# Kernel tuning notes

Hardware: AMD Instinct MI355X
Metric: run time of the kernel (lower is better)

Reference implementation:

```python
import jax, jax.numpy as jnp
import numpy as np

N_NODES = 10000
N_EDGES = 160000
N_GRAPHS = 64
F = 80        # hidden dim
T = 5         # towers
F_OUT = 16    # per-tower post output (80/5)
N_LAYERS = 4
EPS = 1e-6
BN_EPS = 1e-5
STD_EPS = 1e-5


def setup_inputs() -> dict:
    key = jax.random.key(0)
    ks = jax.random.split(key, 12)
    x = jax.random.uniform(ks[0], (N_NODES, 2), dtype=jnp.float32)
    edge_index = jax.random.randint(ks[1], (2, N_EDGES), 0, N_NODES, dtype=jnp.int64)
    batch = jnp.sort(jax.random.randint(ks[2], (N_NODES,), 0, N_GRAPHS, dtype=jnp.int64))

    def w(k, shape, fan_in):
        return (jax.random.normal(k, shape, jnp.float32) / np.float32(np.sqrt(fan_in)))

    return {
        "x": x, "edge_index": edge_index, "batch": batch,
        "pre_lin_W": w(ks[3], (1, F), 1), "pre_lin_b": jnp.zeros((F,), jnp.float32),
        "pre_W": w(ks[4], (N_LAYERS, T, 2 * F, F), 2 * F), "pre_b": jnp.zeros((N_LAYERS, T, F), jnp.float32),
        "post_W": w(ks[5], (N_LAYERS, T, 13 * F, F_OUT), 13 * F), "post_b": jnp.zeros((N_LAYERS, T, F_OUT), jnp.float32),
        "lin_W": w(ks[6], (N_LAYERS, F, F), F), "lin_b": jnp.zeros((N_LAYERS, F), jnp.float32),
        "bn_gamma": jnp.ones((N_LAYERS, F), jnp.float32), "bn_beta": jnp.zeros((N_LAYERS, F), jnp.float32),
        "mlp_lin_W": w(ks[7], (40, 1), 40), "mlp_lin_b": jnp.zeros((1,), jnp.float32),
        "mlp1_W": w(ks[8], (40, 20), 40), "mlp1_b": jnp.zeros((20,), jnp.float32),
        "mlp2_W": w(ks[9], (20, 1), 20), "mlp2_b": jnp.zeros((1,), jnp.float32),
    }


def _pna_conv(h, src, dst, deg, avg_log_deg, preW, preb, postW, postb, linW, linb):
    # h: [N, F]; messages per tower: pre MLP over cat(x_i, x_j)  (divide_input=False)
    N = h.shape[0]
    hm = jnp.concatenate([h[dst], h[src]], axis=-1)            # [E, 2F]
    m = jnp.einsum('ef,tfo->eto', hm, preW) + preb             # [E, T, F]

    cnt = jnp.maximum(deg, 1.0)[:, None, None]                 # [N,1,1]
    has = (deg > 0)[:, None, None]
    s = jax.ops.segment_sum(m, dst, num_segments=N)
    mean = s / cnt
    mean_sq = jax.ops.segment_sum(m * m, dst, num_segments=N) / cnt
    mn = jax.ops.segment_min(m, dst, num_segments=N)
    mx = jax.ops.segment_max(m, dst, num_segments=N)
    mn = jnp.where(has, mn, 0.0)
    mx = jnp.where(has, mx, 0.0)
    std = jnp.sqrt(jax.nn.relu(mean_sq - mean * mean) + STD_EPS)
    agg = jnp.concatenate([mean, mn, mx, std], axis=-1)        # [N, T, 4F]

    logd = jnp.log(jnp.maximum(deg, 1.0) + 1.0)[:, None, None]
    amp = agg * (logd / avg_log_deg)
    att = agg * (avg_log_deg / logd)
    out = jnp.concatenate([agg, amp, att], axis=-1)            # [N, T, 12F]

    xt = jnp.broadcast_to(h[:, None, :], (N, T, F))
    out = jnp.concatenate([xt, out], axis=-1)                  # [N, T, 13F]
    out = jnp.einsum('ntf,tfo->nto', out, postW) + postb       # [N, T, F_OUT]
    out = out.reshape(N, T * F_OUT)                            # [N, 80]
    return out @ linW + linb


def _forward(x, edge_index, batch, pre_lin_W, pre_lin_b, pre_W, pre_b,
             post_W, post_b, lin_W, lin_b, bn_gamma, bn_beta,
             mlp_lin_W, mlp_lin_b, mlp1_W, mlp1_b, mlp2_W, mlp2_b):
    N = x.shape[0]
    src, dst = edge_index[0], edge_index[1]
    deg = jax.ops.segment_sum(jnp.ones_like(dst, jnp.float32), dst, num_segments=N)
    avg_log_deg = jnp.mean(jnp.log(deg + 1.0))                 # PNA avg log-degree from deg histogram

    operation = x[:, 0:1]
    assignment = x[:, 1:2]
    op = operation @ pre_lin_W + pre_lin_b                     # [N, 80]

    for l in range(N_LAYERS):
        y = _pna_conv(op, src, dst, deg, avg_log_deg,
                      pre_W[l], pre_b[l], post_W[l], post_b[l], lin_W[l], lin_b[l])
        mu = jnp.mean(y, axis=0)
        var = jnp.mean((y - mu) ** 2, axis=0)                  # biased, training-mode BN
        y = (y - mu) / jnp.sqrt(var + BN_EPS) * bn_gamma[l] + bn_beta[l]
        op = jax.nn.relu(y)

    front, behind = op[:, :40], op[:, 40:]
    xc = front * assignment + behind                           # [N, 40], non-negative

    # LastLayer: log-space scatter-add message passing
    log_score = jax.ops.segment_sum(jnp.log(xc[src] + EPS), dst, num_segments=N)
    xc = jnp.exp(log_score + jnp.log(xc + EPS))

    # global mean pool over graphs
    gcnt = jnp.maximum(jax.ops.segment_sum(jnp.ones_like(batch, jnp.float32), batch, num_segments=N_GRAPHS), 1.0)
    pooled = jax.ops.segment_sum(xc, batch, num_segments=N_GRAPHS) / gcnt[:, None]  # [B, 40]

    x_lin = pooled @ mlp_lin_W + mlp_lin_b
    x_cv = pooled @ mlp1_W + mlp1_b
    x_cv = 20.0 - jax.nn.relu(x_cv)
    x_cv = x_cv @ mlp2_W + mlp2_b
    return x_cv + x_lin                                        # [B, 1]


def reference(x, edge_index, batch, pre_lin_W, pre_lin_b, pre_W, pre_b,
              post_W, post_b, lin_W, lin_b, bn_gamma, bn_beta,
              mlp_lin_W, mlp_lin_b, mlp1_W, mlp1_b, mlp2_W, mlp2_b):
    return _forward(x, edge_index, batch, pre_lin_W, pre_lin_b, pre_W, pre_b,
                    post_W, post_b, lin_W, lin_b, bn_gamma, bn_beta,
                    mlp_lin_W, mlp_lin_b, mlp1_W, mlp1_b, mlp2_W, mlp2_b)
```

## Files before the change

### kernel.cpp

```cpp
#include <hip/hip_runtime.h>
#include <math.h>

#define NN 10000
#define NE 160000
#define NG 64
#define FEAT 80
#define NT 5
#define NL 4

__global__ void k_cnt2(const int* __restrict__ dst, const int* __restrict__ batch,
                       int* __restrict__ deg, int* __restrict__ gcnt) {
    int e = blockIdx.x * 256 + threadIdx.x;
    if (e < NE) atomicAdd(&deg[dst[e]], 1);
    if (e < NN) atomicAdd(&gcnt[batch[e]], 1);
}

__global__ void k_scan(const int* __restrict__ deg, int* __restrict__ offs) {
    __shared__ int sums[256];
    int tid = threadIdx.x;
    int start = tid * 40, stop = min(start + 40, NN);
    int s = 0;
    for (int i = start; i < stop; ++i) s += deg[i];
    sums[tid] = s;
    __syncthreads();
    for (int off = 1; off < 256; off <<= 1) {
        int v = (tid >= off) ? sums[tid - off] : 0;
        __syncthreads();
        sums[tid] += v;
        __syncthreads();
    }
    int base = (tid == 0) ? 0 : sums[tid - 1];
    for (int i = start; i < stop; ++i) { offs[i] = base; base += deg[i]; }
    if (tid == 255) offs[NN] = sums[255];
}

__global__ void k_ald(const int* __restrict__ deg, float* __restrict__ ald) {
    __shared__ float red[256];
    int i = blockIdx.x * 256 + threadIdx.x;
    red[threadIdx.x] = (i < NN) ? logf((float)deg[i] + 1.0f) : 0.0f;
    __syncthreads();
    for (int s = 128; s > 0; s >>= 1) {
        if (threadIdx.x < s) red[threadIdx.x] += red[threadIdx.x + s];
        __syncthreads();
    }
    if (threadIdx.x == 0) atomicAdd(ald, red[0]);
}

__global__ void k_fill(const int* __restrict__ src, const int* __restrict__ dst,
                       const int* __restrict__ offs, int* __restrict__ cursor,
                       int* __restrict__ csr) {
    int e = blockIdx.x * 256 + threadIdx.x;
    if (e < NE) {
        int d = dst[e];
        int p = atomicAdd(&cursor[d], 1);
        csr[offs[d] + p] = src[e];
    }
}

__global__ void k_op0(const float* __restrict__ x, const float* __restrict__ plW,
                      const float* __restrict__ plb, float* __restrict__ hT) {
    int i = blockIdx.x * 256 + threadIdx.x;
    if (i < FEAT * NN) {
        int f = i / NN, n = i - f * NN;
        hT[i] = x[2 * n] * plW[f] + plb[f];
    }
}

__global__ __launch_bounds__(256) void k_mm_ab(
        const float* __restrict__ hT_in, const float* __restrict__ preW_l,
        float* __restrict__ A, float* __restrict__ Bt,
        const float* __restrict__ yT, const float* __restrict__ bnst_p,
        const float* __restrict__ gamma_p, const float* __restrict__ beta_p,
        float* __restrict__ hT_out, int use_bn) {
    __shared__ float hs[16][80];
    int n0 = blockIdx.x * 16;
    int tid = threadIdx.x;
    for (int i = tid; i < 16 * 80; i += 256) {
        int nl = i & 15, f = i >> 4;
        float v;
        if (use_bn) {
            float y = yT[(size_t)f * NN + n0 + nl];
            float mu = bnst_p[f] * (1.f / NN);
            float msq = bnst_p[80 + f] * (1.f / NN);
            float var = fmaxf(msq - mu * mu, 0.f);
            v = (y - mu) * (1.f / sqrtf(var + 1e-5f)) * gamma_p[f] + beta_p[f];
            v = fmaxf(v, 0.f);
            hT_out[(size_t)f * NN + n0 + nl] = v;
        } else {
            v = hT_in[(size_t)f * NN + n0 + nl];
        }
        hs[nl][f] = v;
    }
    __syncthreads();
    float acc[4][16];
#pragma unroll
    for (int s = 0; s < 4; s++)
#pragma unroll
        for (int i = 0; i < 16; i++) acc[s][i] = 0.f;
    const float* wp[4];
#pragma unroll
    for (int s = 0; s < 4; s++) {
        int c = tid + s * 256;
        int cs = (c < 800) ? c : 0;
        int part = (cs >= 400) ? 1 : 0;
        int cc = cs - part * 400;
        int t = cc / 80, o = cc - t * 80;
        wp[s] = preW_l + (size_t)(t * 160 + part * 80) * 80 + o;
    }
    for (int fq = 0; fq < 80; fq += 4) {
        float w[4][4];
#pragma unroll
        for (int s = 0; s < 4; s++) {
            w[s][0] = wp[s][(fq + 0) * 80];
            w[s][1] = wp[s][(fq + 1) * 80];
            w[s][2] = wp[s][(fq + 2) * 80];
            w[s][3] = wp[s][(fq + 3) * 80];
        }
#pragma unroll
        for (int i = 0; i < 16; i++) {
            float4 hv = *(const float4*)&hs[i][fq];
#pragma unroll
            for (int s = 0; s < 4; s++) {
                acc[s][i] += hv.x * w[s][0] + hv.y * w[s][1] +
                             hv.z * w[s][2] + hv.w * w[s][3];
            }
        }
    }
#pragma unroll
    for (int s = 0; s < 4; s++) {
        int c = tid + s * 256;
        if (c < 800) {
            int part = (c >= 400) ? 1 : 0;
            int cc = c - part * 400;
            int t = cc / 80, o = cc - t * 80;
            if (part == 0) {
#pragma unroll
                for (int i = 0; i < 16; i++) A[(size_t)(n0 + i) * 400 + cc] = acc[s][i];
            } else {
#pragma unroll
                for (int i = 0; i < 16; i++)
                    Bt[((size_t)t * NN + n0 + i) * 80 + o] = acc[s][i];
            }
        }
    }
}

__global__ __launch_bounds__(256) void k_agg_t(
        const float* __restrict__ A, const float* __restrict__ Bt,
        const int* __restrict__ offs, const int* __restrict__ csr,
        const float* __restrict__ preb_l, float* __restrict__ aggT) {
    __shared__ float st[320 * 17];
    int tid = threadIdx.x;
    int id = blockIdx.y * 625 + blockIdx.x;
    int xcd = id & 7;
    int slot = id >> 3;
    int base = (xcd <= 5) ? xcd * 391 : 5 * 391 + (xcd - 5) * 390;
    int r = base + slot;
    int t = r / 625;
    int n0 = (r - t * 625) * 16;
    int ni = tid >> 4;
    int cl = tid & 15;
    int n = n0 + ni;
    int e0 = offs[n], e1 = offs[n + 1];
    const float* Bts = Bt + (size_t)t * NN * 80;
    float s[5], q[5], mn[5], mx[5];
#pragma unroll
    for (int k = 0; k < 5; k++) { s[k] = 0.f; q[k] = 0.f; mn[k] = 3.4e38f; mx[k] = -3.4e38f; }
    int e = e0;
    for (; e + 3 < e1; e += 4) {
        const float* br0 = Bts + (size_t)csr[e] * 80 + cl;
        const float* br1 = Bts + (size_t)csr[e + 1] * 80 + cl;
        const float* br2 = Bts + (size_t)csr[e + 2] * 80 + cl;
        const float* br3 = Bts + (size_t)csr[e + 3] * 80 + cl;
#pragma unroll
        for (int k = 0; k < 5; k++) {
            float b0 = br0[k * 16];
            float b1 = br1[k * 16];
            float b2 = br2[k * 16];
            float b3 = br3[k * 16];
            s[k] += (b0 + b1) + (b2 + b3);
            q[k] += (b0 * b0 + b1 * b1) + (b2 * b2 + b3 * b3);
            mn[k] = fminf(mn[k], fminf(fminf(b0, b1), fminf(b2, b3)));
            mx[k] = fmaxf(mx[k], fmaxf(fmaxf(b0, b1), fmaxf(b2, b3)));
        }
    }
    for (; e < e1; ++e) {
        const float* br = Bts + (size_t)csr[e] * 80 + cl;
#pragma unroll
        for (int k = 0; k < 5; k++) {
            float b = br[k * 16];
            s[k] += b; q[k] += b * b;
            mn[k] = fminf(mn[k], b); mx[k] = fmaxf(mx[k], b);
        }
    }
    int d = e1 - e0;
    float degf = (float)d;
    float cnt = fmaxf(degf, 1.f);
#pragma unroll
    for (int k = 0; k < 5; k++) {
        int c = cl + k * 16;
        float a = A[(size_t)n * 400 + t * 80 + c] + preb_l[t * 80 + c];
        float mean = (degf * a + s[k]) / cnt;
        float msq  = (degf * a * a + 2.f * a * s[k] + q[k]) / cnt;
        float sd = sqrtf(fmaxf(msq - mean * mean, 0.f) + 1e-5f);
        float mnr = (d > 0) ? a + mn[k] : 0.f;
        float mxr = (d > 0) ? a + mx[k] : 0.f;
        st[(0 * 80 + c) * 17 + ni] = mean;
        st[(1 * 80 + c) * 17 + ni] = mnr;
        st[(2 * 80 + c) * 17 + ni] = mxr;
        st[(3 * 80 + c) * 17 + ni] = sd;
    }
    __syncthreads();
    int jj = tid >> 4;
    int nl = tid & 15;
#pragma unroll
    for (int pass = 0; pass < 20; ++pass) {
        int j = pass * 16 + jj;
        aggT[((size_t)t * 320 + j) * NN + n0 + nl] = st[j * 17 + nl];
    }
}

__global__ __launch_bounds__(256) void k_post(
        const float* __restrict__ hT, const float* __restrict__ aggT,
        const float* __restrict__ postW_l, const float* __restrict__ postb_l,
        const int* __restrict__ offs, const float* __restrict__ ald_sum,
        float* __restrict__ y0T) {
    __shared__ float wj[40 * 48];
    __shared__ float wh[80 * 16];
    int tid = threadIdx.x;
    int t = blockIdx.y;
    int jq = blockIdx.z;
    int j0 = jq * 40;
    const float* W0 = postW_l + (size_t)t * 1040 * 16;
    const float* W1 = W0 + 80 * 16;
    const float* W2 = W0 + 400 * 16;
    const float* W3 = W0 + 720 * 16;
    for (int idx = tid; idx < 40 * 48; idx += 256) {
        int j = idx / 48;
        int rem = idx - j * 48;
        int p = rem >> 4, o = rem & 15;
        const float* Wp = (p == 0) ? W1 : (p == 1) ? W2 : W3;
        wj[idx] = Wp[(j0 + j) * 16 + o];
    }
    if (jq == 0) {
        for (int idx = tid; idx < 80 * 16; idx += 256)
            wh[idx] = W0[idx];
    }
    __syncthreads();
    int n = blockIdx.x * 256 + tid;
    bool alive = (n < NN);
    int nc = alive ? n : 0;
    float acc1[16], acc2[16], acc3[16];
#pragma unroll
    for (int i = 0; i < 16; i++) { acc1[i] = 0.f; acc2[i] = 0.f; acc3[i] = 0.f; }
    const float* ap = aggT + ((size_t)t * 320 + j0) * NN + nc;
#pragma unroll 8
    for (int j = 0; j < 40; ++j) {
        float a = ap[(size_t)j * NN];
        const float* w = wj + j * 48;
#pragma unroll
        for (int i = 0; i < 16; i++) {
            acc1[i] += a * w[i];
            acc2[i] += a * w[16 + i];
            acc3[i] += a * w[32 + i];
        }
    }
    if (jq == 0) {
#pragma unroll 4
        for (int f = 0; f < 80; ++f) {
            float hv = hT[(size_t)f * NN + nc];
            const float* w = wh + f * 16;
#pragma unroll
            for (int i = 0; i < 16; i++) acc1[i] += hv * w[i];
        }
    }
    if (alive) {
        float degf = (float)(offs[n + 1] - offs[n]);
        float ald = ald_sum[0] * (1.f / NN);
        float logd = logf(fmaxf(degf, 1.f) + 1.f);
        float c1 = logd / ald;
        float c2 = ald / logd;
#pragma unroll
        for (int i = 0; i < 16; i++) {
            float v = acc1[i] + c1 * acc2[i] + c2 * acc3[i];
            if (jq == 0) v += postb_l[t * 16 + i];
            unsafeAtomicAdd(&y0T[(size_t)(t * 16 + i) * NN + n], v);
        }
    }
}

__global__ __launch_bounds__(256) void k_lin(
        const float* __restrict__ y0T, const float* __restrict__ linW_l,
        const float* __restrict__ linb_l, float* __restrict__ yT) {
    __shared__ float ws[80 * 8];
    int tid = threadIdx.x;
    int f0 = blockIdx.y * 8;
    for (int idx = tid; idx < 80 * 8; idx += 256)
        ws[idx] = linW_l[(idx >> 3) * 80 + f0 + (idx & 7)];
    __syncthreads();
    int n = blockIdx.x * 256 + tid;
    bool alive = (n < NN);
    int nc = alive ? n : 0;
    float acc[8];
#pragma unroll
    for (int i = 0; i < 8; i++) acc[i] = 0.f;
#pragma unroll 8
    for (int k = 0; k < 80; ++k) {
        float v = y0T[(size_t)k * NN + nc];
        const float4 wa = *(const float4*)(ws + k * 8);
        const float4 wb = *(const float4*)(ws + k * 8 + 4);
        acc[0] += v * wa.x; acc[1] += v * wa.y; acc[2] += v * wa.z; acc[3] += v * wa.w;
        acc[4] += v * wb.x; acc[5] += v * wb.y; acc[6] += v * wb.z; acc[7] += v * wb.w;
    }
    if (alive) {
#pragma unroll
        for (int i = 0; i < 8; i++)
            yT[(size_t)(f0 + i) * NN + n] = acc[i] + linb_l[f0 + i];
    }
}

__global__ void k_bnstats(const float* __restrict__ yT, float* __restrict__ bnst) {
    __shared__ float r1[256], r2[256];
    int f = blockIdx.x;
    int seg = blockIdx.y;
    int tid = threadIdx.x;
    int i0 = seg * 1250, i1 = min(i0 + 1250, NN);
    float s = 0.f, q = 0.f;
    for (int i = i0 + tid; i < i1; i += 256) {
        float v = yT[(size_t)f * NN + i];
        s += v; q += v * v;
    }
    r1[tid] = s; r2[tid] = q;
    __syncthreads();
    for (int st = 128; st > 0; st >>= 1) {
        if (tid < st) { r1[tid] += r1[tid + st]; r2[tid] += r2[tid + st]; }
        __syncthreads();
    }
    if (tid == 0) {
        unsafeAtomicAdd(&bnst[f], r1[0]);
        unsafeAtomicAdd(&bnst[80 + f], r2[0]);
    }
}

__global__ void k_bnxc(const float* __restrict__ yT, const float* __restrict__ bnst,
                       const float* __restrict__ gamma_l, const float* __restrict__ beta_l,
                       const float* __restrict__ x, float* __restrict__ lxc) {
    int i = blockIdx.x * 256 + threadIdx.x;
    if (i >= 40 * NN) return;
    int f = i / NN, n = i - f * NN;
    int f2 = f + 40;
    float mu1 = bnst[f] * (1.f / NN);
    float ms1 = bnst[80 + f] * (1.f / NN);
    float v1 = (yT[(size_t)f * NN + n] - mu1) *
               (1.f / sqrtf(fmaxf(ms1 - mu1 * mu1, 0.f) + 1e-5f)) * gamma_l[f] + beta_l[f];
    v1 = fmaxf(v1, 0.f);
    float mu2 = bnst[f2] * (1.f / NN);
    float ms2 = bnst[80 + f2] * (1.f / NN);
    float v2 = (yT[(size_t)f2 * NN + n] - mu2) *
               (1.f / sqrtf(fmaxf(ms2 - mu2 * mu2, 0.f) + 1e-5f)) * gamma_l[f2] + beta_l[f2];
    v2 = fmaxf(v2, 0.f);
    lxc[(size_t)n * 40 + f] = logf(v1 * x[2 * n + 1] + v2 + 1e-6f);
}

__global__ void k_logagg(const float* __restrict__ lxc, const int* __restrict__ offs,
                         const int* __restrict__ csr, const int* __restrict__ batch,
                         float* __restrict__ pooled) {
    int n = blockIdx.x;
    int tid = threadIdx.x;
    if (tid >= 40) return;
    int e0 = offs[n], e1 = offs[n + 1];
    float s = 0.f;
    for (int k = e0; k < e1; ++k) s += lxc[(size_t)csr[k] * 40 + tid];
    float v = expf(s + lxc[(size_t)n * 40 + tid]);
    atomicAdd(&pooled[batch[n] * 40 + tid], v);
}

__global__ void k_final(const float* __restrict__ pooled, const int* __restrict__ gcnt,
                        const float* __restrict__ mlW, const float* __restrict__ mlb,
                        const float* __restrict__ m1W, const float* __restrict__ m1b,
                        const float* __restrict__ m2W, const float* __restrict__ m2b,
                        float* __restrict__ out) {
    int g = threadIdx.x;
    if (g >= NG) return;
    float inv = 1.f / fmaxf((float)gcnt[g], 1.f);
    float pl[40];
#pragma unroll
    for (int j = 0; j < 40; j++) pl[j] = pooled[g * 40 + j] * inv;
    float xl = mlb[0];
#pragma unroll
    for (int j = 0; j < 40; j++) xl += pl[j] * mlW[j];
    float acc = m2b[0];
    for (int k = 0; k < 20; k++) {
        float v = m1b[k];
#pragma unroll
        for (int j = 0; j < 40; j++) v += pl[j] * m1W[j * 20 + k];
        v = 20.f - fmaxf(v, 0.f);
        acc += v * m2W[k];
    }
    out[g] = acc + xl;
}

extern "C" void kernel_launch(void* const* d_in, const int* in_sizes, int n_in,
                              void* d_out, int out_size, void* d_ws, size_t ws_size,
                              hipStream_t stream) {
    const float* x     = (const float*)d_in[0];
    const int*   ei    = (const int*)d_in[1];
    const int*   batch = (const int*)d_in[2];
    const float* plW   = (const float*)d_in[3];
    const float* plb   = (const float*)d_in[4];
    const float* preW  = (const float*)d_in[5];
    const float* preb  = (const float*)d_in[6];
    const float* postW = (const float*)d_in[7];
    const float* postb = (const float*)d_in[8];
    const float* linW  = (const float*)d_in[9];
    const float* linb  = (const float*)d_in[10];
    const float* bnG   = (const float*)d_in[11];
    const float* bnB   = (const float*)d_in[12];
    const float* mlW   = (const float*)d_in[13];
    const float* mlb   = (const float*)d_in[14];
    const float* m1W   = (const float*)d_in[15];
    const float* m1b   = (const float*)d_in[16];
    const float* m2W   = (const float*)d_in[17];
    const float* m2b   = (const float*)d_in[18];
    float* out = (float*)d_out;
    const int* srcp = ei;
    const int* dstp = ei + NE;

    char* p = (char*)d_ws;
    int*   deg    = (int*)(p + 0);
    int*   cursor = (int*)(p + 40000);
    int*   gcnt   = (int*)(p + 80000);
    float* ald    = (float*)(p + 80256);
    float* pooled = (float*)(p + 80272);
    float* bnst   = (float*)(p + 90512);
    int*   offs   = (int*)(p + 93072);
    int*   csr    = (int*)(p + 133088);
    float* hT     = (float*)(p + 773088);
    float* A      = (float*)(p + 3973088);
    float* Bt     = (float*)(p + 19973088);
    float* aggT   = (float*)(p + 35973088);
    float* y0T = (float*)(p + 23173088);
    float* yT  = (float*)(p + 26373088);
    float* lxc = (float*)(p + 35973088);

    hipMemsetAsync(d_ws, 0, 93072, stream);
    k_cnt2<<<dim3((NE + 255) / 256), 256, 0, stream>>>(dstp, batch, deg, gcnt);
    k_scan<<<1, 256, 0, stream>>>(deg, offs);
    k_ald<<<dim3((NN + 255) / 256), 256, 0, stream>>>(deg, ald);
    k_fill<<<dim3((NE + 255) / 256), 256, 0, stream>>>(srcp, dstp, offs, cursor, csr);
    k_op0<<<dim3((FEAT * NN + 255) / 256), 256, 0, stream>>>(x, plW, plb, hT);

    for (int l = 0; l < NL; ++l) {
        const float* preW_l  = preW  + (size_t)l * NT * 160 * 80;
        const float* preb_l  = preb  + l * NT * 80;
        const float* postW_l = postW + (size_t)l * NT * 1040 * 16;
        const float* postb_l = postb + l * NT * 16;
        const float* linW_l  = linW  + l * 80 * 80;
        const float* linb_l  = linb  + l * 80;
        float* bnst_l = bnst + l * 160;
        if (l == 0) {
            k_mm_ab<<<dim3(625), 256, 0, stream>>>(hT, preW_l, A, Bt,
                                                   nullptr, nullptr, nullptr, nullptr,
                                                   nullptr, 0);
        } else {
            k_mm_ab<<<dim3(625), 256, 0, stream>>>(hT, preW_l, A, Bt,
                                                   yT, bnst + (l - 1) * 160,
                                                   bnG + (l - 1) * 80, bnB + (l - 1) * 80,
                                                   hT, 1);
        }
        k_agg_t<<<dim3(625, 5), 256, 0, stream>>>(A, Bt, offs, csr, preb_l, aggT);
        hipMemsetAsync(y0T, 0, (size_t)80 * NN * 4, stream);
        k_post<<<dim3(40, 5, 8), 256, 0, stream>>>(hT, aggT, postW_l, postb_l, offs, ald, y0T);
        k_lin<<<dim3(40, 10), 256, 0, stream>>>(y0T, linW_l, linb_l, yT);
        k_bnstats<<<dim3(80, 8), 256, 0, stream>>>(yT, bnst_l);
        if (l == NL - 1) {
            k_bnxc<<<dim3((40 * NN + 255) / 256), 256, 0, stream>>>(
                yT, bnst_l, bnG + l * 80, bnB + l * 80, x, lxc);
        }
    }

    k_logagg<<<dim3(NN), 64, 0, stream>>>(lxc, offs, csr, batch, pooled);
    k_final<<<1, 64, 0, stream>>>(pooled, gcnt, mlW, mlb, m1W, m1b, m2W, m2b, out);
}
```

Measured before the change: 780.1 us.

## Register-block two nodes per thread in k_post and halve the j-chunk per block

Each thread in the post-aggregation matmul now handles two nodes (na and na+256), so every shared-memory weight read feeds twice as many FMAs. To offset the extra accumulator pressure (96 floats), the j-range per block shrinks from 40 to 20, and the grid becomes 20x5x16. The jq==0 blocks still carry the extra 80-feature h term. Higher register use may lower occupancy, and the doubled z-split doubles the atomic adds into y0T.

Result: slower. 846.6 us (+8.5%).

```diff
diff --git a/kernel.cpp b/kernel.cpp
--- a/kernel.cpp
+++ b/kernel.cpp
@@ -225,17 +225,17 @@
         const float* __restrict__ postW_l, const float* __restrict__ postb_l,
         const int* __restrict__ offs, const float* __restrict__ ald_sum,
         float* __restrict__ y0T) {
-    __shared__ float wj[40 * 48];
+    __shared__ float wj[20 * 48];
     __shared__ float wh[80 * 16];
     int tid = threadIdx.x;
     int t = blockIdx.y;
     int jq = blockIdx.z;
-    int j0 = jq * 40;
+    int j0 = jq * 20;
     const float* W0 = postW_l + (size_t)t * 1040 * 16;
     const float* W1 = W0 + 80 * 16;
     const float* W2 = W0 + 400 * 16;
     const float* W3 = W0 + 720 * 16;
-    for (int idx = tid; idx < 40 * 48; idx += 256) {
+    for (int idx = tid; idx < 20 * 48; idx += 256) {
         int j = idx / 48;
         int rem = idx - j * 48;
         int p = rem >> 4, o = rem & 15;
@@ -247,44 +247,63 @@
             wh[idx] = W0[idx];
     }
     __syncthreads();
-    int n = blockIdx.x * 256 + tid;
-    bool alive = (n < NN);
-    int nc = alive ? n : 0;
-    float acc1[16], acc2[16], acc3[16];
-#pragma unroll
-    for (int i = 0; i < 16; i++) { acc1[i] = 0.f; acc2[i] = 0.f; acc3[i] = 0.f; }
-    const float* ap = aggT + ((size_t)t * 320 + j0) * NN + nc;
-#pragma unroll 8
-    for (int j = 0; j < 40; ++j) {
-        float a = ap[(size_t)j * NN];
+    int na = blockIdx.x * 512 + tid;
+    int nb = na + 256;
+    bool alive_b = (nb < NN);
+    int ncb = alive_b ? nb : na;
+    float accA[48], accB[48];
+#pragma unroll
+    for (int i = 0; i < 48; i++) { accA[i] = 0.f; accB[i] = 0.f; }
+    const float* ap = aggT + ((size_t)t * 320 + j0) * NN;
+#pragma unroll 4
+    for (int j = 0; j < 20; ++j) {
+        float aA = ap[(size_t)j * NN + na];
+        float aB = ap[(size_t)j * NN + ncb];
         const float* w = wj + j * 48;
 #pragma unroll
         for (int i = 0; i < 16; i++) {
-            acc1[i] += a * w[i];
-            acc2[i] += a * w[16 + i];
-            acc3[i] += a * w[32 + i];
+            accA[i]      += aA * w[i];
+            accA[16 + i] += aA * w[16 + i];
+            accA[32 + i] += aA * w[32 + i];
+            accB[i]      += aB * w[i];
+            accB[16 + i] += aB * w[16 + i];
+            accB[32 + i] += aB * w[32 + i];
         }
     }
     if (jq == 0) {
-#pragma unroll 4
+#pragma unroll 2
         for (int f = 0; f < 80; ++f) {
-            float hv = hT[(size_t)f * NN + nc];
+            float hA = hT[(size_t)f * NN + na];
+            float hB = hT[(size_t)f * NN + ncb];
             const float* w = wh + f * 16;
 #pragma unroll
-            for (int i = 0; i < 16; i++) acc1[i] += hv * w[i];
-        }
-    }
-    if (alive) {
-        float degf = (float)(offs[n + 1] - offs[n]);
-        float ald = ald_sum[0] * (1.f / NN);
+            for (int i = 0; i < 16; i++) {
+                accA[i] += hA * w[i];
+                accB[i] += hB * w[i];
+            }
+        }
+    }
+    float ald = ald_sum[0] * (1.f / NN);
+    {
+        float degf = (float)(offs[na + 1] - offs[na]);
         float logd = logf(fmaxf(degf, 1.f) + 1.f);
-        float c1 = logd / ald;
-        float c2 = ald / logd;
+        float c1 = logd / ald, c2 = ald / logd;
 #pragma unroll
         for (int i = 0; i < 16; i++) {
-            float v = acc1[i] + c1 * acc2[i] + c2 * acc3[i];
+            float v = accA[i] + c1 * accA[16 + i] + c2 * accA[32 + i];
             if (jq == 0) v += postb_l[t * 16 + i];
-            unsafeAtomicAdd(&y0T[(size_t)(t * 16 + i) * NN + n], v);
+            unsafeAtomicAdd(&y0T[(size_t)(t * 16 + i) * NN + na], v);
+        }
+    }
+    if (alive_b) {
+        float degf = (float)(offs[nb + 1] - offs[nb]);
+        float logd = logf(fmaxf(degf, 1.f) + 1.f);
+        float c1 = logd / ald, c2 = ald / logd;
+#pragma unroll
+        for (int i = 0; i < 16; i++) {
+            float v = accB[i] + c1 * accB[16 + i] + c2 * accB[32 + i];
+            if (jq == 0) v += postb_l[t * 16 + i];
+            unsafeAtomicAdd(&y0T[(size_t)(t * 16 + i) * NN + nb], v);
         }
     }
 }
@@ -470,7 +489,7 @@
         }
         k_agg_t<<<dim3(625, 5), 256, 0, stream>>>(A, Bt, offs, csr, preb_l, aggT);
         hipMemsetAsync(y0T, 0, (size_t)80 * NN * 4, stream);
-        k_post<<<dim3(40, 5, 8), 256, 0, stream>>>(hT, aggT, postW_l, postb_l, offs, ald, y0T);
+        k_post<<<dim3(20, 5, 16), 256, 0, stream>>>(hT, aggT, postW_l, postb_l, offs, ald, y0T);
         k_lin<<<dim3(40, 10), 256, 0, stream>>>(y0T, linW_l, linb_l, yT);
         k_bnstats<<<dim3(80, 8), 256, 0, stream>>>(yT, bnst_l);
         if (l == NL - 1) {
```
